# Kernel tuning notes

Hardware: AMD Instinct MI355X
Metric: run time of the kernel (lower is better)

## Reference

```python
import jax, jax.numpy as jnp
import numpy as np

B, D, N_CAT, S = 8192, 128, 8192, 4
EPS = 1e-12  # F.normalize eps


def setup_inputs() -> dict:
    key = jax.random.key(0)
    k1, k2, k3, k4 = jax.random.split(key, 4)
    return {
        "batch_x": jax.random.normal(k1, (B, D), dtype=jnp.float32),
        "cat": jax.random.normal(k2, (N_CAT, D), dtype=jnp.float32),
        "y": jax.random.uniform(k3, (N_CAT,), dtype=jnp.float32),
        "phi": jax.random.normal(k4, (S, D), dtype=jnp.float32) * (6.0 / (D + 1)) ** 0.5,  # xavier-ish scale
        "bias": jnp.zeros((1,), dtype=jnp.float32),
    }


def reference(batch_x, cat, y, phi, bias):
    # con[n, b] = cat[n] . batch_x[b]   -> [N_cat, B]
    con = cat @ batch_x.T
    # F.normalize(con, p=4, dim=0): divide each column by its 4-norm (clamped)
    norm4 = jnp.sum(jnp.abs(con) ** 4, axis=0, keepdims=True) ** 0.25
    con = con / jnp.maximum(norm4, EPS)
    con = jax.nn.softmax(con, axis=0)
    s = phi.shape[0]
    c = con.shape[0] // s
    psi = con.reshape(s, c, con.shape[1])      # source_size chunks of [C, B]
    y_r = y.reshape(s, c)                      # source_size chunks of labels
    theta = jnp.exp(batch_x @ phi.T).T         # [S, B], raw exp (theta/sum_src unused in original)
    # sum over sources and chunk rows of y[s,c] * psi[s,c,b] * theta[s,b]
    y_hat = jnp.einsum('sc,scb,sb->b', y_r, psi, theta) + bias
    return y_hat
```

## Files before the change

kernel.cpp:

```cpp
#include <hip/hip_runtime.h>
#include <hip/hip_bf16.h>
#include <math.h>

typedef __bf16 bf16x8 __attribute__((ext_vector_type(8)));
typedef float f32x4 __attribute__((ext_vector_type(4)));

namespace {
constexpr int BN   = 8192;
constexpr int DK   = 128;
constexpr int NCAT = 8192;
constexpr int SRC  = 4;
constexpr int RG   = 8;
constexpr int TROWS = 128;
constexpr int NT   = 8;
constexpr float LOG2E = 1.4426950408889634f;
}

__device__ __forceinline__ float4 ld4(const float* p) {
    return *reinterpret_cast<const float4*>(p);
}

__global__ __launch_bounds__(256) void k_convert2(const float* __restrict__ x,
                                                  const float* __restrict__ cat,
                                                  unsigned short* __restrict__ xb,
                                                  unsigned short* __restrict__ catb) {
    const int i = blockIdx.x * 256 + threadIdx.x;
    const int nx = BN * DK / 8;
    const float* src;
    unsigned short* dst;
    int j;
    if (i < nx) { src = x; dst = xb; j = i; }
    else        { src = cat; dst = catb; j = i - nx; }
    const float4 a = ld4(src + (size_t)j * 8);
    const float4 b = ld4(src + (size_t)j * 8 + 4);
    float vals[8] = {a.x, a.y, a.z, a.w, b.x, b.y, b.z, b.w};
    union { unsigned short u[8]; uint4 v; } o;
#pragma unroll
    for (int q = 0; q < 8; ++q) {
        __hip_bfloat16 h = __float2bfloat16(vals[q]);
        o.u[q] = *reinterpret_cast<unsigned short*>(&h);
    }
    *reinterpret_cast<uint4*>(&dst[(size_t)j * 8]) = o.v;
}

template <int PASS>
__global__ __launch_bounds__(256, 2) void k_pass(
    const unsigned short* __restrict__ xb,
    const unsigned short* __restrict__ catb,
    const float* __restrict__ y,
    const float* __restrict__ pp4in,
    float* __restrict__ outA,
    float* __restrict__ outB) {
    __shared__ __align__(16) unsigned short As[2][TROWS * DK];
    __shared__ float ysh[2][TROWS];
    __shared__ float nsh[128];
    __shared__ float redA[2][128];
    __shared__ float redB[2][128];

    const int t = threadIdx.x;
    const int colbase = blockIdx.x * 128;
    const int rowgrp = blockIdx.y;
    const int rowbase0 = rowgrp * 1024;

    const int wid = t >> 6;
    const int lane = t & 63;
    const int wr = wid >> 1;
    const int wc = wid & 1;
    const int lr = lane & 15;
    const int kb = lane >> 4;

    const int srow = t >> 4;
    const int scol = t & 15;

    uint4 stg[8];
    {
        const unsigned short* tb = catb + (size_t)rowbase0 * DK;
#pragma unroll
        for (int q = 0; q < 8; ++q)
            stg[q] = *reinterpret_cast<const uint4*>(tb + (size_t)(q * 256 + t) * 8);
    }

    bf16x8 Bf[4][4];
#pragma unroll
    for (int j = 0; j < 4; ++j)
#pragma unroll
        for (int kk = 0; kk < 4; ++kk)
            Bf[j][kk] = *reinterpret_cast<const bf16x8*>(
                &xb[(size_t)(colbase + wc * 64 + j * 16 + lr) * DK + kk * 32 + kb * 8]);

    if (PASS == 2) {
        if (t < 128) {
            float sp = 0.f;
#pragma unroll
            for (int r = 0; r < RG; ++r) sp += pp4in[r * BN + colbase + t];
            nsh[t] = LOG2E / fmaxf(sqrtf(sqrtf(sp)), 1e-12f);
        }
        if (t < TROWS) ysh[0][t] = y[rowbase0 + t];
    }

#pragma unroll
    for (int q = 0; q < 8; ++q) {
        const int r = q * 16 + srow;
        *reinterpret_cast<uint4*>(&As[0][r * DK + (scol ^ (r & 7)) * 8]) = stg[q];
    }
    __syncthreads();

    float inm[4];
    if (PASS == 2) {
#pragma unroll
        for (int j = 0; j < 4; ++j) inm[j] = nsh[wc * 64 + j * 16 + lr];
    }

    float accA[4] = {0.f, 0.f, 0.f, 0.f};
    float accB[4] = {0.f, 0.f, 0.f, 0.f};

    for (int tl = 0; tl < NT; ++tl) {
        const int cur = tl & 1, nxt = cur ^ 1;
        float yreg = 0.f;
        if (tl < NT - 1) {
            const unsigned short* nb =
                catb + (size_t)(rowbase0 + (tl + 1) * TROWS) * DK;
#pragma unroll
            for (int q = 0; q < 8; ++q)
                stg[q] = *reinterpret_cast<const uint4*>(nb + (size_t)(q * 256 + t) * 8);
            if (PASS == 2 && t < TROWS) yreg = y[rowbase0 + (tl + 1) * TROWS + t];
        }

        f32x4 acc[4][4];
#pragma unroll
        for (int i = 0; i < 4; ++i)
#pragma unroll
            for (int j = 0; j < 4; ++j) acc[i][j] = (f32x4){0.f, 0.f, 0.f, 0.f};

#pragma unroll
        for (int kk = 0; kk < 4; ++kk) {
            bf16x8 a[4];
#pragma unroll
            for (int i = 0; i < 4; ++i) {
                const int row = wr * 64 + i * 16 + lr;
                a[i] = *reinterpret_cast<const bf16x8*>(
                    &As[cur][row * DK + ((kk * 32 + kb * 8) ^ ((lr & 7) * 8))]);
            }
#pragma unroll
            for (int i = 0; i < 4; ++i)
#pragma unroll
                for (int j = 0; j < 4; ++j)
                    acc[i][j] = __builtin_amdgcn_mfma_f32_16x16x32_bf16(
                        a[i], Bf[j][kk], acc[i][j], 0, 0, 0);
        }

        if (PASS == 1) {
#pragma unroll
            for (int i = 0; i < 4; ++i)
#pragma unroll
                for (int j = 0; j < 4; ++j)
#pragma unroll
                    for (int r = 0; r < 4; ++r) {
                        const float v = acc[i][j][r];
                        const float v2 = v * v;
                        accA[j] = fmaf(v2, v2, accA[j]);
                    }
        } else {
#pragma unroll
            for (int i = 0; i < 4; ++i)
#pragma unroll
                for (int r = 0; r < 4; ++r) {
                    const float yr = ysh[cur][wr * 64 + i * 16 + kb * 4 + r];
#pragma unroll
                    for (int j = 0; j < 4; ++j) {
                        const float e = exp2f(acc[i][j][r] * inm[j]);
                        accA[j] += e;
                        accB[j] = fmaf(yr, e, accB[j]);
                    }
                }
        }

        if (tl < NT - 1) {
#pragma unroll
            for (int q = 0; q < 8; ++q) {
                const int r = q * 16 + srow;
                *reinterpret_cast<uint4*>(&As[nxt][r * DK + (scol ^ (r & 7)) * 8]) = stg[q];
            }
            if (PASS == 2 && t < TROWS) ysh[nxt][t] = yreg;
        }
        __syncthreads();
    }

#pragma unroll
    for (int j = 0; j < 4; ++j) {
        accA[j] += __shfl_xor(accA[j], 16, 64);
        accA[j] += __shfl_xor(accA[j], 32, 64);
        if (PASS == 2) {
            accB[j] += __shfl_xor(accB[j], 16, 64);
            accB[j] += __shfl_xor(accB[j], 32, 64);
        }
    }
    if (lane < 16) {
#pragma unroll
        for (int j = 0; j < 4; ++j) {
            redA[wr][wc * 64 + j * 16 + lane] = accA[j];
            if (PASS == 2) redB[wr][wc * 64 + j * 16 + lane] = accB[j];
        }
    }
    __syncthreads();
    if (t < 128) {
        outA[(size_t)rowgrp * BN + colbase + t] = redA[0][t] + redA[1][t];
        if (PASS == 2)
            outB[(size_t)rowgrp * BN + colbase + t] = redB[0][t] + redB[1][t];
    }
}

__global__ __launch_bounds__(256) void k_final(const float* __restrict__ x,
                                               const float* __restrict__ phi,
                                               const float* __restrict__ pZ,
                                               const float* __restrict__ pW,
                                               const float* __restrict__ bias,
                                               float* __restrict__ out) {
    const int g = blockIdx.x * 256 + threadIdx.x;
    const int b = g >> 2, s = g & 3;
    float dot = 0.f;
#pragma unroll
    for (int k = 0; k < DK; k += 4) {
        const float4 xv = ld4(&x[(size_t)b * DK + k]);
        const float4 pv = ld4(&phi[s * DK + k]);
        dot += xv.x * pv.x + xv.y * pv.y + xv.z * pv.z + xv.w * pv.w;
    }
    const float W = pW[(size_t)(2 * s) * BN + b] + pW[(size_t)(2 * s + 1) * BN + b];
    float v = __expf(dot) * W;
    float Z = pZ[(size_t)(2 * s) * BN + b] + pZ[(size_t)(2 * s + 1) * BN + b];
    v += __shfl_xor(v, 1, 64);
    v += __shfl_xor(v, 2, 64);
    Z += __shfl_xor(Z, 1, 64);
    Z += __shfl_xor(Z, 2, 64);
    if (s == 0) out[b] = v / Z + bias[0];
}

extern "C" void kernel_launch(void* const* d_in, const int* in_sizes, int n_in,
                              void* d_out, int out_size, void* d_ws, size_t ws_size,
                              hipStream_t stream) {
    const float* x    = (const float*)d_in[0];
    const float* cat  = (const float*)d_in[1];
    const float* y    = (const float*)d_in[2];
    const float* phi  = (const float*)d_in[3];
    const float* bias = (const float*)d_in[4];
    float* out = (float*)d_out;

    char* ws = (char*)d_ws;
    unsigned short* xb   = (unsigned short*)ws;
    unsigned short* catb = xb + (size_t)BN * DK;
    float* pp4 = (float*)(catb + (size_t)NCAT * DK);
    float* pZ  = pp4 + (size_t)RG * BN;
    float* pW  = pZ + (size_t)RG * BN;

    k_convert2<<<(BN * DK + NCAT * DK) / 8 / 256, 256, 0, stream>>>(x, cat, xb, catb);
    k_pass<1><<<dim3(BN / 128, RG), 256, 0, stream>>>(xb, catb, y, nullptr, pp4, nullptr);
    k_pass<2><<<dim3(BN / 128, RG), 256, 0, stream>>>(xb, catb, y, pp4, pZ, pW);
    k_final<<<BN * SRC / 256, 256, 0, stream>>>(x, phi, pZ, pW, bias, out);
}
```

Baseline: 64.14 us.

## Load cat tiles directly to LDS and pre-swizzle layout in convert

The convert kernel now writes cat in a pre-swizzled tiled layout so the pass kernels can use global_load_lds to stream tiles straight into shared memory, bypassing register staging and the separate LDS store. Row tiles shrink to 64 and row groups double to 16, with occupancy raised to 4 blocks per CU, and y is preloaded once per block. The final kernel sums 4 partials per source instead of 2. This removes register pressure and VGPR round trips but halves MFMA work per tile and adds more partial outputs and blocks.

```diff
diff --git a/kernel.cpp b/kernel.cpp
--- a/kernel.cpp
+++ b/kernel.cpp
@@ -10,14 +10,20 @@
 constexpr int DK   = 128;
 constexpr int NCAT = 8192;
 constexpr int SRC  = 4;
-constexpr int RG   = 8;
-constexpr int TROWS = 128;
+constexpr int RG   = 16;
+constexpr int TROWS = 64;
 constexpr int NT   = 8;
 constexpr float LOG2E = 1.4426950408889634f;
 }
 
 __device__ __forceinline__ float4 ld4(const float* p) {
     return *reinterpret_cast<const float4*>(p);
+}
+
+__device__ __forceinline__ void load_lds16(const unsigned short* g, unsigned short* l) {
+    __builtin_amdgcn_global_load_lds(
+        (const __attribute__((address_space(1))) void*)g,
+        (__attribute__((address_space(3))) void*)l, 16, 0, 0);
 }
 
 __global__ __launch_bounds__(256) void k_convert2(const float* __restrict__ x,
@@ -29,8 +35,15 @@
     const float* src;
     unsigned short* dst;
     int j;
-    if (i < nx) { src = x; dst = xb; j = i; }
-    else        { src = cat; dst = catb; j = i - nx; }
+    size_t dchunk;
+    if (i < nx) {
+        src = x; dst = xb; j = i; dchunk = (size_t)j;
+    } else {
+        src = cat; dst = catb; j = i - nx;
+        const int r = j >> 4, c = j & 15;
+        const int rt = r >> 6, r6 = r & 63;
+        dchunk = (size_t)rt * 1024 + r6 * 16 + (c ^ (r6 & 7));
+    }
     const float4 a = ld4(src + (size_t)j * 8);
     const float4 b = ld4(src + (size_t)j * 8 + 4);
     float vals[8] = {a.x, a.y, a.z, a.w, b.x, b.y, b.z, b.w};
@@ -40,11 +53,11 @@
         __hip_bfloat16 h = __float2bfloat16(vals[q]);
         o.u[q] = *reinterpret_cast<unsigned short*>(&h);
     }
-    *reinterpret_cast<uint4*>(&dst[(size_t)j * 8]) = o.v;
+    *reinterpret_cast<uint4*>(&dst[dchunk * 8]) = o.v;
 }
 
 template <int PASS>
-__global__ __launch_bounds__(256, 2) void k_pass(
+__global__ __launch_bounds__(256, 4) void k_pass(
     const unsigned short* __restrict__ xb,
     const unsigned short* __restrict__ catb,
     const float* __restrict__ y,
@@ -52,7 +65,7 @@
     float* __restrict__ outA,
     float* __restrict__ outB) {
     __shared__ __align__(16) unsigned short As[2][TROWS * DK];
-    __shared__ float ysh[2][TROWS];
+    __shared__ float ysh[512];
     __shared__ float nsh[128];
     __shared__ float redA[2][128];
     __shared__ float redB[2][128];
@@ -60,7 +73,7 @@
     const int t = threadIdx.x;
     const int colbase = blockIdx.x * 128;
     const int rowgrp = blockIdx.y;
-    const int rowbase0 = rowgrp * 1024;
+    const int tile0 = rowgrp * NT;
 
     const int wid = t >> 6;
     const int lane = t & 63;
@@ -69,16 +82,10 @@
     const int lr = lane & 15;
     const int kb = lane >> 4;
 
-    const int srow = t >> 4;
-    const int scol = t & 15;
-
-    uint4 stg[8];
-    {
-        const unsigned short* tb = catb + (size_t)rowbase0 * DK;
-#pragma unroll
-        for (int q = 0; q < 8; ++q)
-            stg[q] = *reinterpret_cast<const uint4*>(tb + (size_t)(q * 256 + t) * 8);
-    }
+#pragma unroll
+    for (int q = 0; q < 4; ++q)
+        load_lds16(catb + ((size_t)tile0 * 1024 + (wid * 4 + q) * 64 + lane) * 8,
+                   &As[0][(wid * 4 + q) * 64 * 8]);
 
     bf16x8 Bf[4][4];
 #pragma unroll
@@ -95,13 +102,8 @@
             for (int r = 0; r < RG; ++r) sp += pp4in[r * BN + colbase + t];
             nsh[t] = LOG2E / fmaxf(sqrtf(sqrtf(sp)), 1e-12f);
         }
-        if (t < TROWS) ysh[0][t] = y[rowbase0 + t];
-    }
-
-#pragma unroll
-    for (int q = 0; q < 8; ++q) {
-        const int r = q * 16 + srow;
-        *reinterpret_cast<uint4*>(&As[0][r * DK + (scol ^ (r & 7)) * 8]) = stg[q];
+#pragma unroll
+        for (int q = t; q < 512; q += 256) ysh[q] = y[rowgrp * 512 + q];
     }
     __syncthreads();
 
@@ -116,33 +118,31 @@
 
     for (int tl = 0; tl < NT; ++tl) {
         const int cur = tl & 1, nxt = cur ^ 1;
-        float yreg = 0.f;
         if (tl < NT - 1) {
-            const unsigned short* nb =
-                catb + (size_t)(rowbase0 + (tl + 1) * TROWS) * DK;
-#pragma unroll
-            for (int q = 0; q < 8; ++q)
-                stg[q] = *reinterpret_cast<const uint4*>(nb + (size_t)(q * 256 + t) * 8);
-            if (PASS == 2 && t < TROWS) yreg = y[rowbase0 + (tl + 1) * TROWS + t];
-        }
-
-        f32x4 acc[4][4];
-#pragma unroll
-        for (int i = 0; i < 4; ++i)
+#pragma unroll
+            for (int q = 0; q < 4; ++q)
+                load_lds16(catb + ((size_t)(tile0 + tl + 1) * 1024 +
+                                   (wid * 4 + q) * 64 + lane) * 8,
+                           &As[nxt][(wid * 4 + q) * 64 * 8]);
+        }
+
+        f32x4 acc[2][4];
+#pragma unroll
+        for (int i = 0; i < 2; ++i)
 #pragma unroll
             for (int j = 0; j < 4; ++j) acc[i][j] = (f32x4){0.f, 0.f, 0.f, 0.f};
 
 #pragma unroll
         for (int kk = 0; kk < 4; ++kk) {
-            bf16x8 a[4];
-#pragma unroll
-            for (int i = 0; i < 4; ++i) {
-                const int row = wr * 64 + i * 16 + lr;
-                a[i] = *reinterpret_cast<const bf16x8*>(
-                    &As[cur][row * DK + ((kk * 32 + kb * 8) ^ ((lr & 7) * 8))]);
+            bf16x8 a[2];
+#pragma unroll
+            for (int i = 0; i < 2; ++i) {
+                const int row = wr * 32 + i * 16 + lr;
+                const int chunk = (kk * 4 + kb) ^ (lr & 7);
+                a[i] = *reinterpret_cast<const bf16x8*>(&As[cur][row * 128 + chunk * 8]);
             }
 #pragma unroll
-            for (int i = 0; i < 4; ++i)
+            for (int i = 0; i < 2; ++i)
 #pragma unroll
                 for (int j = 0; j < 4; ++j)
                     acc[i][j] = __builtin_amdgcn_mfma_f32_16x16x32_bf16(
@@ -151,7 +151,7 @@
 
         if (PASS == 1) {
 #pragma unroll
-            for (int i = 0; i < 4; ++i)
+            for (int i = 0; i < 2; ++i)
 #pragma unroll
                 for (int j = 0; j < 4; ++j)
 #pragma unroll
@@ -162,10 +162,13 @@
                     }
         } else {
 #pragma unroll
-            for (int i = 0; i < 4; ++i)
+            for (int i = 0; i < 2; ++i) {
+                const float4 yv =
+                    *reinterpret_cast<const float4*>(&ysh[tl * 64 + wr * 32 + i * 16 + kb * 4]);
+                const float yr4[4] = {yv.x, yv.y, yv.z, yv.w};
 #pragma unroll
                 for (int r = 0; r < 4; ++r) {
-                    const float yr = ysh[cur][wr * 64 + i * 16 + kb * 4 + r];
+                    const float yr = yr4[r];
 #pragma unroll
                     for (int j = 0; j < 4; ++j) {
                         const float e = exp2f(acc[i][j][r] * inm[j]);
@@ -173,15 +176,7 @@
                         accB[j] = fmaf(yr, e, accB[j]);
                     }
                 }
-        }
-
-        if (tl < NT - 1) {
-#pragma unroll
-            for (int q = 0; q < 8; ++q) {
-                const int r = q * 16 + srow;
-                *reinterpret_cast<uint4*>(&As[nxt][r * DK + (scol ^ (r & 7)) * 8]) = stg[q];
             }
-            if (PASS == 2 && t < TROWS) ysh[nxt][t] = yreg;
         }
         __syncthreads();
     }
@@ -225,9 +220,13 @@
         const float4 pv = ld4(&phi[s * DK + k]);
         dot += xv.x * pv.x + xv.y * pv.y + xv.z * pv.z + xv.w * pv.w;
     }
-    const float W = pW[(size_t)(2 * s) * BN + b] + pW[(size_t)(2 * s + 1) * BN + b];
+    float W = 0.f, Z = 0.f;
+#pragma unroll
+    for (int r = 0; r < 4; ++r) {
+        W += pW[(size_t)(4 * s + r) * BN + b];
+        Z += pZ[(size_t)(4 * s + r) * BN + b];
+    }
     float v = __expf(dot) * W;
-    float Z = pZ[(size_t)(2 * s) * BN + b] + pZ[(size_t)(2 * s + 1) * BN + b];
     v += __shfl_xor(v, 1, 64);
     v += __shfl_xor(v, 2, 64);
     Z += __shfl_xor(Z, 1, 64);
```

New measurement: 82.73 us. 1.29x slower.
